# Kernel optimization log

Measured on AMD Instinct MI355X. Metric: run time of the kernel, lower is better.

Reference implementation:

```python
import jax, jax.numpy as jnp
import numpy as np
from jax.scipy.special import logsumexp
from jax.scipy.linalg import solve_triangular

STATE_DIM = 64
OBS_DIM = 32
NUM_PARTICLES = 32768
T = 64
DT = 0.01
DAMPING = 0.99
TEMPERATURE = 0.5
LOG_2PI = float(np.log(2.0 * np.pi))


def setup_inputs() -> dict:
    key = jax.random.key(0)
    ks = jax.random.split(key, 6)
    observations = jax.random.normal(ks[0], (T + 1, OBS_DIM), dtype=jnp.float32)
    A = 0.1 * jax.random.normal(ks[1], (STATE_DIM, STATE_DIM), dtype=jnp.float32)
    C = 0.1 * jax.random.normal(ks[2], (OBS_DIM, STATE_DIM), dtype=jnp.float32)
    Q_terms = 0.01 * jax.random.normal(ks[3], (STATE_DIM, STATE_DIM, STATE_DIM), dtype=jnp.float32)
    # torch init: eye * 0.1; add small perturbation so gradients are non-trivial
    Q_chol = 0.1 * jnp.eye(STATE_DIM, dtype=jnp.float32) + 0.005 * jax.random.normal(ks[4], (STATE_DIM, STATE_DIM), dtype=jnp.float32)
    R_chol = 0.1 * jnp.eye(OBS_DIM, dtype=jnp.float32) + 0.005 * jax.random.normal(ks[5], (OBS_DIM, OBS_DIM), dtype=jnp.float32)
    return {"observations": observations, "A": A, "C": C, "Q_terms": Q_terms,
            "Q_chol": Q_chol, "R_chol": R_chol}


def _obs_log_prob(particles, obs, C, L_R):
    """MVN log p(obs | C @ x, R) for each particle. particles [N,D], obs [obs_dim]."""
    mean = particles @ C.T                       # [N, obs_dim]
    diff = obs[None, :] - mean                   # [N, obs_dim]
    z = solve_triangular(L_R, diff.T, lower=True)  # [obs_dim, N]
    log_det_half = jnp.sum(jnp.log(jnp.diag(L_R)))
    return -0.5 * (OBS_DIM * LOG_2PI + jnp.sum(z * z, axis=0)) - log_det_half


def _smc_forward(observations, A, C, Q_terms, Q_chol, R_chol):
    R = R_chol @ R_chol.T
    L_R = jnp.linalg.cholesky(R)

    key = jax.random.key(42)
    k_init, k_scan = jax.random.split(key)
    particles = jax.random.normal(k_init, (NUM_PARTICLES, STATE_DIM), dtype=jnp.float32)
    log_weights = _obs_log_prob(particles, observations[0], C, L_R)

    def step(carry, xs):
        particles, log_weights, lml = carry
        obs_t, t = xs
        k = jax.random.fold_in(k_scan, t)
        k1, k2 = jax.random.split(k)

        log_w = log_weights - logsumexp(log_weights)
        u = jax.random.uniform(k1, (NUM_PARTICLES,), dtype=jnp.float32)
        gumbel = -jnp.log(-jnp.log(u + 1e-10) + 1e-10)
        ancestor_probs = jax.nn.softmax((log_w + gumbel) / TEMPERATURE)
        # Faithful to torch broadcast: collapses to the weighted-mean particle [1, D]
        resampled = (ancestor_probs @ particles)[None, :]

        noise = jax.random.normal(k2, (NUM_PARTICLES, STATE_DIM), dtype=jnp.float32) @ Q_chol.T
        quad = jnp.einsum('ijk,bj,bk->bi', Q_terms, resampled, resampled)  # [1, D]
        mean = resampled + DT * (resampled @ A.T + quad) * DAMPING          # [1, D]
        new_particles = mean + noise                                        # [N, D]

        new_log_weights = _obs_log_prob(new_particles, obs_t, C, L_R)
        new_lml = lml + logsumexp(new_log_weights)
        return (new_particles, new_log_weights, new_lml), None

    init = (particles, log_weights, jnp.zeros((), dtype=jnp.float32))
    (_, _, lml), _ = jax.lax.scan(step, init, (observations[1:], jnp.arange(T)))
    return lml[None]  # shape (1,) like torch


def reference(observations, A, C, Q_terms, Q_chol, R_chol):
    return _smc_forward(observations, A, C, Q_terms, Q_chol, R_chol)
```

## Files before the change

kernel.cpp:

```cpp
#include <hip/hip_runtime.h>
#include <cstdint>

#define NPART 32768
#define HALFN 16384

#define WS_W     0
#define WS_M     2048
#define WS_B     4096
#define WS_C0    6176
#define WS_KI    6178
#define WS_NK    6180
#define WS_UK    6308
#define WS_P4    6440
#define WS_PSE   8488
#define WS_QP64  24872
#define WS_END   25384

#define ATS32(p, v) __hip_atomic_store((p), (v), __ATOMIC_RELAXED, __HIP_MEMORY_SCOPE_AGENT)
#define ATL32(p)    __hip_atomic_load((p), __ATOMIC_RELAXED, __HIP_MEMORY_SCOPE_AGENT)
#define ATS64(p, v) __hip_atomic_store((p), (v), __ATOMIC_RELAXED, __HIP_MEMORY_SCOPE_AGENT)
#define ATL64(p)    __hip_atomic_load((p), __ATOMIC_RELAXED, __HIP_MEMORY_SCOPE_AGENT)

struct HK { uint32_t a, b; };

__host__ __device__ inline HK tf2x32(uint32_t k0, uint32_t k1, uint32_t x0, uint32_t x1) {
  uint32_t kx = k0 ^ k1 ^ 0x1BD11BDAu;
#define TF_R(r) { x0 += x1; x1 = (x1 << (r)) | (x1 >> (32 - (r))); x1 ^= x0; }
  x0 += k0; x1 += k1;
  TF_R(13) TF_R(15) TF_R(26) TF_R(6)
  x0 += k1; x1 += kx + 1u;
  TF_R(17) TF_R(29) TF_R(16) TF_R(24)
  x0 += kx; x1 += k0 + 2u;
  TF_R(13) TF_R(15) TF_R(26) TF_R(6)
  x0 += k0; x1 += k1 + 3u;
  TF_R(17) TF_R(29) TF_R(16) TF_R(24)
  x0 += k1; x1 += kx + 4u;
  TF_R(13) TF_R(15) TF_R(26) TF_R(6)
  x0 += kx; x1 += k0 + 5u;
#undef TF_R
  HK r; r.a = x0; r.b = x1; return r;
}

__device__ inline float erfinv_f(float x) {
  float w = -log1pf(-x * x);
  float p;
  if (w < 5.0f) {
    w -= 2.5f;
    p = 2.81022636e-08f;
    p = fmaf(p, w, 3.43273939e-07f);
    p = fmaf(p, w, -3.5233877e-06f);
    p = fmaf(p, w, -4.39150654e-06f);
    p = fmaf(p, w, 0.00021858087f);
    p = fmaf(p, w, -0.00125372503f);
    p = fmaf(p, w, -0.00417768164f);
    p = fmaf(p, w, 0.246640727f);
    p = fmaf(p, w, 1.50140941f);
  } else {
    w = sqrtf(w) - 3.0f;
    p = -0.000200214257f;
    p = fmaf(p, w, 0.000100950558f);
    p = fmaf(p, w, 0.00134934322f);
    p = fmaf(p, w, -0.00367342844f);
    p = fmaf(p, w, 0.00573950773f);
    p = fmaf(p, w, -0.0076224613f);
    p = fmaf(p, w, 0.00943887047f);
    p = fmaf(p, w, 1.00167406f);
    p = fmaf(p, w, 2.83297682f);
  }
  return p * x;
}

__device__ inline float u01(uint32_t bits) {
  return __uint_as_float((bits >> 9) | 0x3f800000u) - 1.0f;
}

__device__ inline uint64_t packfs(float v, uint32_t sq) {
  return ((uint64_t)sq << 32) | (uint64_t)__float_as_uint(v);
}

__global__ __launch_bounds__(1024) void kp_kernel(float* __restrict__ ws,
    const float* __restrict__ obs, const float* __restrict__ Cm,
    const float* __restrict__ Qc, const float* __restrict__ Rc) {
  __shared__ float Ls[32][32];
  __shared__ float Li[32][32];
  __shared__ float Wsh[32][64];
  const int tid = threadIdx.x;
  const int i = tid >> 5, j = tid & 31;
  uint32_t* wsu = (uint32_t*)ws;
  for (int idx = WS_P4 + tid; idx < WS_END; idx += 1024) wsu[idx] = 0u;
  if (tid <= 64) {
    HK p0 = tf2x32(0u, 42u, 0u, 2u);
    HK p1 = tf2x32(0u, 42u, 1u, 3u);
    uint32_t ks0 = p0.b, ks1 = p1.b;
    HK f = tf2x32(ks0, ks1, 0u, (uint32_t)tid);
    HK q0 = tf2x32(f.a, f.b, 0u, 2u);
    HK q1 = tf2x32(f.a, f.b, 1u, 3u);
    wsu[WS_UK + 2 * tid] = q0.a; wsu[WS_UK + 2 * tid + 1] = q1.a;
    if (tid < 64) { wsu[WS_NK + 2 * tid] = q0.b; wsu[WS_NK + 2 * tid + 1] = q1.b; }
    if (tid == 0) { wsu[WS_KI] = p0.a; wsu[WS_KI + 1] = p1.a; }
  }
  {
    float a = 0.0f;
    for (int k = 0; k < 32; ++k) a = fmaf(Rc[i * 32 + k], Rc[j * 32 + k], a);
    Ls[i][j] = a;
  }
  __syncthreads();
  for (int k = 0; k < 32; ++k) {
    if (tid == 0) Ls[k][k] = sqrtf(Ls[k][k]);
    __syncthreads();
    if (tid > k && tid < 32) Ls[tid][k] /= Ls[k][k];
    __syncthreads();
    if (i > k && j > k && j <= i) Ls[i][j] = fmaf(-Ls[i][k], Ls[j][k], Ls[i][j]);
    __syncthreads();
  }
  if (tid < 32) {
    for (int r = 0; r < 32; ++r) Li[r][tid] = 0.0f;
    Li[tid][tid] = 1.0f / Ls[tid][tid];
    for (int r = tid + 1; r < 32; ++r) {
      float s = 0.0f;
      for (int m = tid; m < r; ++m) s = fmaf(Ls[r][m], Li[m][tid], s);
      Li[r][tid] = -s / Ls[r][r];
    }
  }
  __syncthreads();
  if (tid == 0) {
    float ld = 0.0f;
    for (int k = 0; k < 32; ++k) ld += logf(Ls[k][k]);
    ws[WS_C0] = -0.5f * 32.0f * 1.8378770664093453f - ld;
  }
  for (int idx = tid; idx < 2048; idx += 1024) {
    int o = idx >> 6, d = idx & 63;
    float a = 0.0f;
    for (int k = 0; k < 32; ++k) a = fmaf(Li[o][k], Cm[k * 64 + d], a);
    Wsh[o][d] = a;
    ws[WS_W + idx] = a;
  }
  __syncthreads();
  for (int idx = tid; idx < 2048; idx += 1024) {
    int o = idx >> 6, d = idx & 63;
    float a = 0.0f;
    for (int k = 0; k < 64; ++k) a = fmaf(Wsh[o][k], Qc[k * 64 + d], a);
    ws[WS_M + idx] = a;
  }
  for (int idx = tid; idx < 2080; idx += 1024) {
    int t = idx >> 5, o = idx & 31;
    float a = 0.0f;
    for (int k = 0; k < 32; ++k) a = fmaf(Li[o][k], obs[t * 32 + k], a);
    ws[WS_B + idx] = a;
  }
}

__global__ __launch_bounds__(512, 2) void kmain_kernel(
    float* __restrict__ ws, const float* __restrict__ Am,
    const float* __restrict__ Qcg, const float* __restrict__ Qt,
    float* __restrict__ dout) {
  __shared__ __align__(16) float Ms[2048];
  __shared__ __align__(16) float Wm[2048];
  __shared__ __align__(16) float As[4096];
  __shared__ __align__(16) float Qcs[4096];
  __shared__ __align__(16) float Qs[1024];
  __shared__ float hC[32];
  __shared__ float rS[64], uS[64], mnS[64];
  __shared__ float ebL[256];
  __shared__ float redA[256], redB[256];
  __shared__ float SEw[8][64];
  __shared__ float wred[8][4];
  __shared__ float sc[8];
  __shared__ uint32_t keyL[260];

  const int tid = threadIdx.x;
  const int bid = blockIdx.x;
  uint32_t* wsu = (uint32_t*)ws;
  uint64_t* p4 = (uint64_t*)(ws + WS_P4);
  uint64_t* qp64 = (uint64_t*)(ws + WS_QP64);

  for (int i = tid; i < 2048; i += 512) { Ms[i] = ws[WS_M + i]; Wm[i] = ws[WS_W + i]; }
  for (int i = tid; i < 4096; i += 512) { As[i] = Am[i]; Qcs[i] = Qcg[i]; }
  {
    const int i0 = (bid >> 2) * 4096 + (bid & 3) * 1024;
    for (int i = tid; i < 1024; i += 512) Qs[i] = Qt[i0 + i];
  }
  for (int i = tid; i < 128; i += 512) keyL[i] = wsu[WS_NK + i];
  for (int i = tid; i < 130; i += 512) keyL[128 + i] = wsu[WS_UK + i];
  if (tid == 0) { keyL[258] = wsu[WS_KI]; keyL[259] = wsu[WS_KI + 1]; sc[4] = 0.0f; }
  if (tid < 32) hC[tid] = ws[WS_B + tid];
  const float C0 = ws[WS_C0];
  __syncthreads();

  const int pr = tid >> 3;
  const int l8 = tid & 7;
  const int p = bid * 64 + pr;
  const int d0 = l8 * 8;
  const int wv = tid >> 6, ln = tid & 63;

  float Elo[8], Ehi[8], gl, gh;
  float aL[4], aH[4];

  auto poll64 = [&](uint64_t* pp, uint32_t sq) -> float {
    uint64_t q;
    for (;;) {
      q = ATL64(pp);
      if ((uint32_t)(q >> 32) >= sq) break;
      __builtin_amdgcn_s_sleep(1);
    }
    return __uint_as_float((uint32_t)q);
  };

  auto genE8 = [&](uint32_t k0, uint32_t k1) {
    const uint32_t fb = (uint32_t)(p * 64 + d0);
#pragma unroll
    for (int j = 0; j < 8; ++j) {
      HK o = tf2x32(k0, k1, fb + (uint32_t)j, fb + (uint32_t)j + 1048576u);
      float fl = u01(o.a), fh = u01(o.b);
      float ul = fmaxf(-0.99999994f, fmaf(fl, 2.0f, -0.99999994f));
      float uh = fmaxf(-0.99999994f, fmaf(fh, 2.0f, -0.99999994f));
      Elo[j] = 1.41421354f * erfinv_f(ul);
      Ehi[j] = 1.41421354f * erfinv_f(uh);
    }
  };
  auto genG = [&](uint32_t k0, uint32_t k1) {
    HK og = tf2x32(k0, k1, (uint32_t)p, (uint32_t)(p + 16384));
    gl = -logf(-logf(u01(og.a) + 1e-10f) + 1e-10f);
    gh = -logf(-logf(u01(og.b) + 1e-10f) + 1e-10f);
  };

  auto ringME = [&](const float* matL) {
#pragma unroll
    for (int q = 0; q < 4; ++q) { aL[q] = 0.f; aH[q] = 0.f; }
#pragma unroll
    for (int k = 0; k < 8; ++k) {
      if (k) {
#pragma unroll
        for (int q = 0; q < 4; ++q) {
          aL[q] = __shfl(aL[q], (l8 + 1) & 7, 8);
          aH[q] = __shfl(aH[q], (l8 + 1) & 7, 8);
        }
      }
      const int ow = ((l8 + k) & 7) * 4;
#pragma unroll
      for (int q = 0; q < 4; ++q) {
        const float* mr = matL + (ow + q) * 64 + d0;
        float4 m0 = *(const float4*)mr;
        float4 m1 = *(const float4*)(mr + 4);
        float t0 = aL[q];
        t0 = fmaf(m0.x, Elo[0], t0); t0 = fmaf(m0.y, Elo[1], t0);
        t0 = fmaf(m0.z, Elo[2], t0); t0 = fmaf(m0.w, Elo[3], t0);
        t0 = fmaf(m1.x, Elo[4], t0); t0 = fmaf(m1.y, Elo[5], t0);
        t0 = fmaf(m1.z, Elo[6], t0); t0 = fmaf(m1.w, Elo[7], t0);
        aL[q] = t0;
        float t1 = aH[q];
        t1 = fmaf(m0.x, Ehi[0], t1); t1 = fmaf(m0.y, Ehi[1], t1);
        t1 = fmaf(m0.z, Ehi[2], t1); t1 = fmaf(m0.w, Ehi[3], t1);
        t1 = fmaf(m1.x, Ehi[4], t1); t1 = fmaf(m1.y, Ehi[5], t1);
        t1 = fmaf(m1.z, Ehi[6], t1); t1 = fmaf(m1.w, Ehi[7], t1);
        aH[q] = t1;
      }
    }
  };

  auto tailStore = [&](uint32_t sq) {
    const int ob = ((l8 + 7) & 7) * 4;
    float s2l = 0.f, s2h = 0.f;
#pragma unroll
    for (int q = 0; q < 4; ++q) {
      float zl = hC[ob + q] - aL[q], zh = hC[ob + q] - aH[q];
      s2l = fmaf(zl, zl, s2l); s2h = fmaf(zh, zh, s2h);
    }
#pragma unroll
    for (int m = 1; m < 8; m <<= 1) { s2l += __shfl_xor(s2l, m, 8); s2h += __shfl_xor(s2h, m, 8); }
    const float lwL = C0 - 0.5f * s2l, lwH = C0 - 0.5f * s2h;
    const float yl = (lwL + gl) * 2.0f, yh = (lwH + gh) * 2.0f;
    float mv = fmaxf(yl, yh), ml = fmaxf(lwL, lwH);
#pragma unroll
    for (int m = 1; m < 64; m <<= 1) {
      mv = fmaxf(mv, __shfl_xor(mv, m, 64));
      ml = fmaxf(ml, __shfl_xor(ml, m, 64));
    }
    if (ln == 0) { wred[wv][0] = mv; wred[wv][1] = ml; }
    __syncthreads();
    if (tid == 0) {
      float a = wred[0][0], b = wred[0][1];
      for (int q = 1; q < 8; ++q) { a = fmaxf(a, wred[q][0]); b = fmaxf(b, wred[q][1]); }
      sc[0] = a; sc[1] = b;
    }
    __syncthreads();
    const float myb = sc[0], mlb = sc[1];
    const float wLo = expf(yl - myb), wHi = expf(yh - myb);
    float vzy = (l8 == 0) ? (wLo + wHi) : 0.0f;
    float vzl = (l8 == 0) ? (expf(lwL - mlb) + expf(lwH - mlb)) : 0.0f;
#pragma unroll
    for (int m = 1; m < 64; m <<= 1) { vzy += __shfl_xor(vzy, m, 64); vzl += __shfl_xor(vzl, m, 64); }
    if (ln == 0) { wred[wv][2] = vzy; wred[wv][3] = vzl; }
    float v[8];
#pragma unroll
    for (int j = 0; j < 8; ++j) v[j] = fmaf(wHi, Ehi[j], wLo * Elo[j]);
#pragma unroll
    for (int m = 8; m < 64; m <<= 1) {
#pragma unroll
      for (int j = 0; j < 8; ++j) v[j] += __shfl_xor(v[j], m, 64);
    }
    if (ln < 8) {
#pragma unroll
      for (int j = 0; j < 8; ++j) SEw[wv][ln * 8 + j] = v[j];
    }
    __syncthreads();
    if (tid < 64) {
      float ssum = SEw[0][tid];
      for (int q = 1; q < 8; ++q) ssum += SEw[q][tid];
      ATS32(ws + WS_PSE + (bid << 6) + tid, ssum);
    }
    if (tid < 64) asm volatile("s_waitcnt vmcnt(0)" ::: "memory");
    if (tid == 0) {
      float zy = wred[0][2], zl2 = wred[0][3];
      for (int q = 1; q < 8; ++q) { zy += wred[q][2]; zl2 += wred[q][3]; }
      uint64_t* bp = p4 + bid * 4;
      ATS64(bp + 0, packfs(myb, sq));
      ATS64(bp + 1, packfs(mlb, sq));
      ATS64(bp + 2, packfs(zy, sq));
      ATS64(bp + 3, packfs(zl2, sq));
    }
  };

  auto combine = [&](int s) {
    const uint32_t sq = (uint32_t)(s + 1);
    float pmv = 0.f, pml = 0.f, pzyv = 0.f, pzlv = 0.f;
    if (tid < 256) {
      uint64_t* bp = p4 + tid * 4;
      pmv = poll64(bp + 0, sq);
      pml = poll64(bp + 1, sq);
      pzyv = poll64(bp + 2, sq);
      pzlv = poll64(bp + 3, sq);
      redA[tid] = pmv; redB[tid] = pml;
    }
    __syncthreads();
    asm volatile("" ::: "memory");
    float pse[32];
    {
      const int d = tid & 63, c = tid >> 6;
#pragma unroll
      for (int b8 = 0; b8 < 32; ++b8)
        pse[b8] = ATL32(ws + WS_PSE + (((c << 5) + b8) << 6) + d);
    }
    for (int st = 128; st > 0; st >>= 1) {
      if (tid < st) {
        redA[tid] = fmaxf(redA[tid], redA[tid + st]);
        redB[tid] = fmaxf(redB[tid], redB[tid + st]);
      }
      __syncthreads();
    }
    const float myg = redA[0], mlwg = redB[0];
    __syncthreads();
    if (tid < 256) {
      float e = expf(pmv - myg);
      ebL[tid] = e;
      redA[tid] = e * pzyv;
      redB[tid] = expf(pml - mlwg) * pzlv;
    }
    __syncthreads();
    for (int st = 128; st > 0; st >>= 1) {
      if (tid < st) { redA[tid] += redA[tid + st]; redB[tid] += redB[tid + st]; }
      __syncthreads();
    }
    if (tid == 0) {
      sc[2] = redA[0];
      if (s > 0) sc[4] += mlwg + logf(redB[0]);
    }
    __syncthreads();
    const float Zy = sc[2];
    {
      const int d = tid & 63, c = tid >> 6;
      float pp = 0.0f;
#pragma unroll
      for (int b8 = 0; b8 < 32; ++b8)
        pp = fmaf(ebL[(c << 5) + b8], pse[b8], pp);
      SEw[c][d] = pp;
    }
    __syncthreads();
    if (tid < 64) {
      float sg = SEw[0][tid];
      for (int c = 1; c < 8; ++c) sg += SEw[c][tid];
      uS[tid] = sg / Zy;
    }
    __syncthreads();
    if (tid < 64) {
      float r;
      if (s == 0) r = uS[tid];
      else {
        r = mnS[tid];
        const float* qr = Qcs + tid * 64;
        for (int k2 = 0; k2 < 64; ++k2) r = fmaf(uS[k2], qr[k2], r);
      }
      rS[tid] = r;
    }
    __syncthreads();
    if (tid < 256) {
      const int jl = tid >> 4, kc = tid & 15;
      const float* qr = Qs + jl * 64 + kc * 4;
      float t0 = qr[0] * rS[kc * 4];
      t0 = fmaf(qr[1], rS[kc * 4 + 1], t0);
      t0 = fmaf(qr[2], rS[kc * 4 + 2], t0);
      t0 = fmaf(qr[3], rS[kc * 4 + 3], t0);
      redA[tid] = t0 * rS[(bid & 3) * 16 + jl];
    }
    __syncthreads();
    for (int st = 128; st > 0; st >>= 1) {
      if (tid < st) redA[tid] += redA[tid + st];
      __syncthreads();
    }
    if (tid == 0) ATS64(qp64 + bid, packfs(redA[0], sq));
  };

  auto meanH = [&](int s) {
    const uint32_t sq = (uint32_t)(s + 1);
    if (tid < 64) {
      uint64_t* qb = qp64 + tid * 4;
      float q0 = poll64(qb + 0, sq);
      float q1 = poll64(qb + 1, sq);
      float q2 = poll64(qb + 2, sq);
      float q3 = poll64(qb + 3, sq);
      float qd = q0 + q1 + q2 + q3;
      float ar = 0.0f;
      const float* arow = As + tid * 64;
      for (int k2 = 0; k2 < 64; ++k2) ar = fmaf(arow[k2], rS[k2], ar);
      mnS[tid] = rS[tid] + 0.0099f * (ar + qd);
    }
    __syncthreads();
    asm volatile("" ::: "memory");
    if (tid < 32) {
      float hv = ws[WS_B + (s + 1) * 32 + tid];
      const float* wrow = Wm + tid * 64;
      for (int d = 0; d < 64; ++d) hv = fmaf(-wrow[d], mnS[d], hv);
      hC[tid] = hv;
    }
    __syncthreads();
  };

  genE8(keyL[258], keyL[259]);
  genG(keyL[128], keyL[129]);
  ringME(Wm);
  tailStore(1u);

  for (int s = 0; s < 64; ++s) {
    genE8(keyL[2 * s], keyL[2 * s + 1]);
    genG(keyL[128 + 2 * (s + 1)], keyL[128 + 2 * (s + 1) + 1]);
    ringME(Ms);
    combine(s);
    meanH(s);
    tailStore((uint32_t)(s + 2));
  }

  {
    const uint32_t sq = 65u;
    float pml = 0.f, pzlv = 0.f;
    if (tid < 256) {
      uint64_t* bp = p4 + tid * 4;
      pml = poll64(bp + 1, sq);
      pzlv = poll64(bp + 3, sq);
      redB[tid] = pml;
    }
    __syncthreads();
    for (int st = 128; st > 0; st >>= 1) {
      if (tid < st) redB[tid] = fmaxf(redB[tid], redB[tid + st]);
      __syncthreads();
    }
    const float mlwg = redB[0];
    __syncthreads();
    if (tid < 256) redB[tid] = expf(pml - mlwg) * pzlv;
    __syncthreads();
    for (int st = 128; st > 0; st >>= 1) {
      if (tid < st) redB[tid] += redB[tid + st];
      __syncthreads();
    }
    if (tid == 0 && bid == 0) dout[0] = sc[4] + mlwg + logf(redB[0]);
  }
}

extern "C" void kernel_launch(void* const* d_in, const int* in_sizes, int n_in,
                              void* d_out, int out_size, void* d_ws, size_t ws_size,
                              hipStream_t stream) {
  const float* obs = (const float*)d_in[0];
  const float* Am = (const float*)d_in[1];
  const float* Cm = (const float*)d_in[2];
  const float* Qt = (const float*)d_in[3];
  const float* Qc = (const float*)d_in[4];
  const float* Rc = (const float*)d_in[5];
  float* ws = (float*)d_ws;
  float* out = (float*)d_out;
  (void)in_sizes; (void)n_in; (void)out_size; (void)ws_size;

  kp_kernel<<<dim3(1), dim3(1024), 0, stream>>>(ws, obs, Cm, Qc, Rc);

  void* params[] = { (void*)&ws, (void*)&Am, (void*)&Qc, (void*)&Qt, (void*)&out };
  hipLaunchCooperativeKernel((const void*)kmain_kernel, dim3(256), dim3(512),
                             params, 0, stream);
}
```

Measured before the change: 1.399 ms.

## Centralize per-step combine in block 0 and broadcast resampled mean via flags

Previously every block polled all 256 blocks' partial sums and redundantly computed the global weighted mean and its Q_chol transform. Now only block 0 does that combine, publishes the resulting vector r to a workspace buffer and sets per-block ready flags, while the other blocks wait on their own flag and read r. The final log-likelihood reduction is also restricted to block 0, and the quadratic-term poll uses a longer sleep. This is meant to cut redundant global memory polling traffic and work, at the cost of an extra serialized publish/wait hop on each step's critical path.

```diff
diff --git a/kernel.cpp b/kernel.cpp
--- a/kernel.cpp
+++ b/kernel.cpp
@@ -14,7 +14,9 @@
 #define WS_P4    6440
 #define WS_PSE   8488
 #define WS_QP64  24872
-#define WS_END   25384
+#define WS_RBUF  25384
+#define WS_RST   25448
+#define WS_END   26472
 
 #define ATS32(p, v) __hip_atomic_store((p), (v), __ATOMIC_RELAXED, __HIP_MEMORY_SCOPE_AGENT)
 #define ATL32(p)    __hip_atomic_load((p), __ATOMIC_RELAXED, __HIP_MEMORY_SCOPE_AGENT)
@@ -173,9 +175,11 @@
   uint32_t* wsu = (uint32_t*)ws;
   uint64_t* p4 = (uint64_t*)(ws + WS_P4);
   uint64_t* qp64 = (uint64_t*)(ws + WS_QP64);
+  uint32_t* rst = wsu + WS_RST;
 
   for (int i = tid; i < 2048; i += 512) { Ms[i] = ws[WS_M + i]; Wm[i] = ws[WS_W + i]; }
-  for (int i = tid; i < 4096; i += 512) { As[i] = Am[i]; Qcs[i] = Qcg[i]; }
+  for (int i = tid; i < 4096; i += 512) As[i] = Am[i];
+  if (bid == 0) for (int i = tid; i < 4096; i += 512) Qcs[i] = Qcg[i];
   {
     const int i0 = (bid >> 2) * 4096 + (bid & 3) * 1024;
     for (int i = tid; i < 1024; i += 512) Qs[i] = Qt[i0 + i];
@@ -202,6 +206,15 @@
       q = ATL64(pp);
       if ((uint32_t)(q >> 32) >= sq) break;
       __builtin_amdgcn_s_sleep(1);
+    }
+    return __uint_as_float((uint32_t)q);
+  };
+  auto poll64b = [&](uint64_t* pp, uint32_t sq) -> float {
+    uint64_t q;
+    for (;;) {
+      q = ATL64(pp);
+      if ((uint32_t)(q >> 32) >= sq) break;
+      __builtin_amdgcn_s_sleep(4);
     }
     return __uint_as_float((uint32_t)q);
   };
@@ -321,7 +334,7 @@
     }
   };
 
-  auto combine = [&](int s) {
+  auto combA = [&](int s) {
     const uint32_t sq = (uint32_t)(s + 1);
     float pmv = 0.f, pml = 0.f, pzyv = 0.f, pzlv = 0.f;
     if (tid < 256) {
@@ -391,8 +404,26 @@
         for (int k2 = 0; k2 < 64; ++k2) r = fmaf(uS[k2], qr[k2], r);
       }
       rS[tid] = r;
-    }
-    __syncthreads();
+      ATS32(ws + WS_RBUF + tid, r);
+    }
+    if (tid < 64) asm volatile("s_waitcnt vmcnt(0)" ::: "memory");
+    __syncthreads();
+    if (tid < 256) ATS32(rst + tid * 4, sq);
+  };
+
+  auto getR = [&](int s) {
+    const uint32_t sq = (uint32_t)(s + 1);
+    if (tid == 0) {
+      while (ATL32(rst + bid * 4) < sq) __builtin_amdgcn_s_sleep(1);
+    }
+    __syncthreads();
+    asm volatile("" ::: "memory");
+    if (tid < 64) rS[tid] = ATL32(ws + WS_RBUF + tid);
+    __syncthreads();
+  };
+
+  auto quadPub = [&](int s) {
+    const uint32_t sq = (uint32_t)(s + 1);
     if (tid < 256) {
       const int jl = tid >> 4, kc = tid & 15;
       const float* qr = Qs + jl * 64 + kc * 4;
@@ -414,10 +445,10 @@
     const uint32_t sq = (uint32_t)(s + 1);
     if (tid < 64) {
       uint64_t* qb = qp64 + tid * 4;
-      float q0 = poll64(qb + 0, sq);
-      float q1 = poll64(qb + 1, sq);
-      float q2 = poll64(qb + 2, sq);
-      float q3 = poll64(qb + 3, sq);
+      float q0 = poll64b(qb + 0, sq);
+      float q1 = poll64b(qb + 1, sq);
+      float q2 = poll64b(qb + 2, sq);
+      float q3 = poll64b(qb + 3, sq);
       float qd = q0 + q1 + q2 + q3;
       float ar = 0.0f;
       const float* arow = As + tid * 64;
@@ -444,12 +475,13 @@
     genE8(keyL[2 * s], keyL[2 * s + 1]);
     genG(keyL[128 + 2 * (s + 1)], keyL[128 + 2 * (s + 1) + 1]);
     ringME(Ms);
-    combine(s);
+    if (bid == 0) combA(s); else getR(s);
+    quadPub(s);
     meanH(s);
     tailStore((uint32_t)(s + 2));
   }
 
-  {
+  if (bid == 0) {
     const uint32_t sq = 65u;
     float pml = 0.f, pzlv = 0.f;
     if (tid < 256) {
@@ -471,7 +503,7 @@
       if (tid < st) redB[tid] += redB[tid + st];
       __syncthreads();
     }
-    if (tid == 0 && bid == 0) dout[0] = sc[4] + mlwg + logf(redB[0]);
+    if (tid == 0) dout[0] = sc[4] + mlwg + logf(redB[0]);
   }
 }
 
```

After: 1.478 ms. +5.6%, slower.

## Cut cross-block sync cost: single-flag partial publish, wave-shuffle reductions

Applied to the files above, without the earlier changes.

Per-block partials now go out as plain 32-bit stores followed by one sequence-tagged 64-bit flag, so consumers poll a single word per block instead of four. The shared-memory tree reductions with many __syncthreads are replaced by single-wave shuffle reductions. The quad-term publish is split out, and the meanH poll is moved after the A·r product with a batched __all spin. Only block 0 now runs the final reduction. The trade-off is a release-ordering assumption: the plain stores must become visible before the flag, which relies on s_waitcnt placement.

```diff
diff --git a/kernel.cpp b/kernel.cpp
--- a/kernel.cpp
+++ b/kernel.cpp
@@ -162,7 +162,7 @@
   __shared__ float hC[32];
   __shared__ float rS[64], uS[64], mnS[64];
   __shared__ float ebL[256];
-  __shared__ float redA[256], redB[256];
+  __shared__ float redA[256], redB[256], redC[256], redD[256];
   __shared__ float SEw[8][64];
   __shared__ float wred[8][4];
   __shared__ float sc[8];
@@ -171,7 +171,6 @@
   const int tid = threadIdx.x;
   const int bid = blockIdx.x;
   uint32_t* wsu = (uint32_t*)ws;
-  uint64_t* p4 = (uint64_t*)(ws + WS_P4);
   uint64_t* qp64 = (uint64_t*)(ws + WS_QP64);
 
   for (int i = tid; i < 2048; i += 512) { Ms[i] = ws[WS_M + i]; Wm[i] = ws[WS_W + i]; }
@@ -304,71 +303,76 @@
       for (int j = 0; j < 8; ++j) SEw[wv][ln * 8 + j] = v[j];
     }
     __syncthreads();
+    float zl2 = 0.0f;
     if (tid < 64) {
       float ssum = SEw[0][tid];
       for (int q = 1; q < 8; ++q) ssum += SEw[q][tid];
       ATS32(ws + WS_PSE + (bid << 6) + tid, ssum);
     }
+    if (tid == 0) {
+      float zy = wred[0][2];
+      zl2 = wred[0][3];
+      for (int q = 1; q < 8; ++q) { zy += wred[q][2]; zl2 += wred[q][3]; }
+      float* pb = ws + WS_P4 + (bid << 3);
+      ATS32(pb + 0, sc[0]);
+      ATS32(pb + 1, sc[1]);
+      ATS32(pb + 2, zy);
+    }
     if (tid < 64) asm volatile("s_waitcnt vmcnt(0)" ::: "memory");
-    if (tid == 0) {
-      float zy = wred[0][2], zl2 = wred[0][3];
-      for (int q = 1; q < 8; ++q) { zy += wred[q][2]; zl2 += wred[q][3]; }
-      uint64_t* bp = p4 + bid * 4;
-      ATS64(bp + 0, packfs(myb, sq));
-      ATS64(bp + 1, packfs(mlb, sq));
-      ATS64(bp + 2, packfs(zy, sq));
-      ATS64(bp + 3, packfs(zl2, sq));
-    }
+    if (tid == 0)
+      ATS64((uint64_t*)(ws + WS_P4 + (bid << 3) + 4), packfs(zl2, sq));
   };
 
   auto combine = [&](int s) {
     const uint32_t sq = (uint32_t)(s + 1);
-    float pmv = 0.f, pml = 0.f, pzyv = 0.f, pzlv = 0.f;
     if (tid < 256) {
-      uint64_t* bp = p4 + tid * 4;
-      pmv = poll64(bp + 0, sq);
-      pml = poll64(bp + 1, sq);
-      pzyv = poll64(bp + 2, sq);
-      pzlv = poll64(bp + 3, sq);
-      redA[tid] = pmv; redB[tid] = pml;
-    }
-    __syncthreads();
-    asm volatile("" ::: "memory");
+      float* pb = ws + WS_P4 + (tid << 3);
+      float zl = poll64((uint64_t*)(pb + 4), sq);
+      asm volatile("" ::: "memory");
+      redA[tid] = ATL32(pb + 0);
+      redB[tid] = ATL32(pb + 1);
+      redC[tid] = ATL32(pb + 2);
+      redD[tid] = zl;
+    }
+    __syncthreads();
     float pse[32];
-    {
-      const int d = tid & 63, c = tid >> 6;
-#pragma unroll
-      for (int b8 = 0; b8 < 32; ++b8)
-        pse[b8] = ATL32(ws + WS_PSE + (((c << 5) + b8) << 6) + d);
-    }
-    for (int st = 128; st > 0; st >>= 1) {
-      if (tid < st) {
-        redA[tid] = fmaxf(redA[tid], redA[tid + st]);
-        redB[tid] = fmaxf(redB[tid], redB[tid + st]);
-      }
-      __syncthreads();
-    }
-    const float myg = redA[0], mlwg = redB[0];
-    __syncthreads();
-    if (tid < 256) {
-      float e = expf(pmv - myg);
-      ebL[tid] = e;
-      redA[tid] = e * pzyv;
-      redB[tid] = expf(pml - mlwg) * pzlv;
-    }
-    __syncthreads();
-    for (int st = 128; st > 0; st >>= 1) {
-      if (tid < st) { redA[tid] += redA[tid + st]; redB[tid] += redB[tid + st]; }
-      __syncthreads();
-    }
-    if (tid == 0) {
-      sc[2] = redA[0];
-      if (s > 0) sc[4] += mlwg + logf(redB[0]);
+    const int d = tid & 63, c = tid >> 6;
+#pragma unroll
+    for (int b8 = 0; b8 < 32; ++b8)
+      pse[b8] = ATL32(ws + WS_PSE + (((c << 5) + b8) << 6) + d);
+    if (tid < 64) {
+      const int l = tid;
+      float a0 = redA[l], a1 = redA[l + 64], a2 = redA[l + 128], a3 = redA[l + 192];
+      float b0 = redB[l], b1 = redB[l + 64], b2 = redB[l + 128], b3 = redB[l + 192];
+      float myg = fmaxf(fmaxf(a0, a2), fmaxf(a1, a3));
+      float mlg = fmaxf(fmaxf(b0, b2), fmaxf(b1, b3));
+#pragma unroll
+      for (int m = 32; m >= 1; m >>= 1) {
+        myg = fmaxf(myg, __shfl_xor(myg, m, 64));
+        mlg = fmaxf(mlg, __shfl_xor(mlg, m, 64));
+      }
+      myg = __shfl(myg, 0, 64); mlg = __shfl(mlg, 0, 64);
+      float zy0 = redC[l], zy1 = redC[l + 64], zy2 = redC[l + 128], zy3 = redC[l + 192];
+      float zl0 = redD[l], zl1 = redD[l + 64], zl2 = redD[l + 128], zl3 = redD[l + 192];
+      float e0 = expf(a0 - myg), e1 = expf(a1 - myg), e2 = expf(a2 - myg), e3 = expf(a3 - myg);
+      ebL[l] = e0; ebL[l + 64] = e1; ebL[l + 128] = e2; ebL[l + 192] = e3;
+      float zyS = (e0 * zy0 + e2 * zy2) + (e1 * zy1 + e3 * zy3);
+      float f0 = expf(b0 - mlg) * zl0, f1 = expf(b1 - mlg) * zl1;
+      float f2 = expf(b2 - mlg) * zl2, f3 = expf(b3 - mlg) * zl3;
+      float zlS = (f0 + f2) + (f1 + f3);
+#pragma unroll
+      for (int m = 32; m >= 1; m >>= 1) {
+        zyS += __shfl_xor(zyS, m, 64);
+        zlS += __shfl_xor(zlS, m, 64);
+      }
+      if (l == 0) {
+        sc[2] = zyS;
+        if (s > 0) sc[4] += mlg + logf(zlS);
+      }
     }
     __syncthreads();
     const float Zy = sc[2];
     {
-      const int d = tid & 63, c = tid >> 6;
       float pp = 0.0f;
 #pragma unroll
       for (int b8 = 0; b8 < 32; ++b8)
@@ -378,7 +382,7 @@
     __syncthreads();
     if (tid < 64) {
       float sg = SEw[0][tid];
-      for (int c = 1; c < 8; ++c) sg += SEw[c][tid];
+      for (int cc = 1; cc < 8; ++cc) sg += SEw[cc][tid];
       uS[tid] = sg / Zy;
     }
     __syncthreads();
@@ -393,6 +397,10 @@
       rS[tid] = r;
     }
     __syncthreads();
+  };
+
+  auto quadPub = [&](int s) {
+    const uint32_t sq = (uint32_t)(s + 1);
     if (tid < 256) {
       const int jl = tid >> 4, kc = tid & 15;
       const float* qr = Qs + jl * 64 + kc * 4;
@@ -403,25 +411,33 @@
       redA[tid] = t0 * rS[(bid & 3) * 16 + jl];
     }
     __syncthreads();
-    for (int st = 128; st > 0; st >>= 1) {
-      if (tid < st) redA[tid] += redA[tid + st];
-      __syncthreads();
-    }
-    if (tid == 0) ATS64(qp64 + bid, packfs(redA[0], sq));
+    if (tid < 64) {
+      float q0 = redA[tid], q1 = redA[tid + 64], q2 = redA[tid + 128], q3 = redA[tid + 192];
+      float qs = (q0 + q2) + (q1 + q3);
+#pragma unroll
+      for (int m = 32; m >= 1; m >>= 1) qs += __shfl_xor(qs, m, 64);
+      if (tid == 0) ATS64(qp64 + bid, packfs(qs, sq));
+    }
   };
 
   auto meanH = [&](int s) {
     const uint32_t sq = (uint32_t)(s + 1);
     if (tid < 64) {
-      uint64_t* qb = qp64 + tid * 4;
-      float q0 = poll64(qb + 0, sq);
-      float q1 = poll64(qb + 1, sq);
-      float q2 = poll64(qb + 2, sq);
-      float q3 = poll64(qb + 3, sq);
-      float qd = q0 + q1 + q2 + q3;
       float ar = 0.0f;
       const float* arow = As + tid * 64;
       for (int k2 = 0; k2 < 64; ++k2) ar = fmaf(arow[k2], rS[k2], ar);
+      uint64_t* qb = qp64 + (tid << 2);
+      uint64_t u0, u1, u2, u3;
+      for (;;) {
+        u0 = ATL64(qb + 0); u1 = ATL64(qb + 1);
+        u2 = ATL64(qb + 2); u3 = ATL64(qb + 3);
+        bool ok = ((uint32_t)(u0 >> 32) >= sq) && ((uint32_t)(u1 >> 32) >= sq) &&
+                  ((uint32_t)(u2 >> 32) >= sq) && ((uint32_t)(u3 >> 32) >= sq);
+        if (__all(ok)) break;
+        __builtin_amdgcn_s_sleep(1);
+      }
+      float qd = __uint_as_float((uint32_t)u0) + __uint_as_float((uint32_t)u1) +
+                 __uint_as_float((uint32_t)u2) + __uint_as_float((uint32_t)u3);
       mnS[tid] = rS[tid] + 0.0099f * (ar + qd);
     }
     __syncthreads();
@@ -429,7 +445,7 @@
     if (tid < 32) {
       float hv = ws[WS_B + (s + 1) * 32 + tid];
       const float* wrow = Wm + tid * 64;
-      for (int d = 0; d < 64; ++d) hv = fmaf(-wrow[d], mnS[d], hv);
+      for (int d2 = 0; d2 < 64; ++d2) hv = fmaf(-wrow[d2], mnS[d2], hv);
       hC[tid] = hv;
     }
     __syncthreads();
@@ -445,17 +461,19 @@
     genG(keyL[128 + 2 * (s + 1)], keyL[128 + 2 * (s + 1) + 1]);
     ringME(Ms);
     combine(s);
+    quadPub(s);
     meanH(s);
     tailStore((uint32_t)(s + 2));
   }
 
-  {
+  if (bid == 0) {
     const uint32_t sq = 65u;
     float pml = 0.f, pzlv = 0.f;
     if (tid < 256) {
-      uint64_t* bp = p4 + tid * 4;
-      pml = poll64(bp + 1, sq);
-      pzlv = poll64(bp + 3, sq);
+      float* pb = ws + WS_P4 + (tid << 3);
+      pzlv = poll64((uint64_t*)(pb + 4), sq);
+      asm volatile("" ::: "memory");
+      pml = ATL32(pb + 1);
       redB[tid] = pml;
     }
     __syncthreads();
@@ -471,7 +489,7 @@
       if (tid < st) redB[tid] += redB[tid + st];
       __syncthreads();
     }
-    if (tid == 0 && bid == 0) dout[0] = sc[4] + mlwg + logf(redB[0]);
+    if (tid == 0) dout[0] = sc[4] + mlwg + logf(redB[0]);
   }
 }
 
```

After: 1.230 ms. 1.14x faster.
